# Kernel tuning notes

Hardware: AMD Instinct MI355X
Metric: run time of the kernel (lower is better)

Reference implementation:

```python
import jax, jax.numpy as jnp
import numpy as np

N_NODES = 100000
N_EDGES = 1200000
IN_DIM = 128
HID = 64
BATCH = 8192


def setup_inputs() -> dict:
    key = jax.random.key(0)
    ks = jax.random.split(key, 8)
    x = jax.random.normal(ks[0], (N_NODES, IN_DIM), dtype=jnp.float32)
    edge_index = jax.random.randint(ks[1], (2, N_EDGES), 0, N_NODES, dtype=jnp.int64)
    user_nodes = jax.random.randint(ks[2], (BATCH,), 0, N_NODES, dtype=jnp.int64)
    movie_nodes = jax.random.randint(ks[3], (BATCH,), 0, N_NODES, dtype=jnp.int64)
    # Glorot-like init for weights, zeros for biases (as in GCNConv / nn.Linear defaults)
    W1 = jax.random.normal(ks[4], (HID, IN_DIM), dtype=jnp.float32) * (1.0 / np.sqrt(IN_DIM))
    b1 = jnp.zeros((HID,), dtype=jnp.float32)
    W2 = jax.random.normal(ks[5], (HID, HID), dtype=jnp.float32) * (1.0 / np.sqrt(HID))
    b2 = jnp.zeros((HID,), dtype=jnp.float32)
    fc_w = jax.random.normal(ks[6], (1, HID), dtype=jnp.float32) * (1.0 / np.sqrt(HID))
    fc_b = jnp.zeros((1,), dtype=jnp.float32)
    return {"x": x, "edge_index": edge_index, "user_nodes": user_nodes,
            "movie_nodes": movie_nodes, "W1": W1, "b1": b1, "W2": W2, "b2": b2,
            "fc_w": fc_w, "fc_b": fc_b}


def _gcn_conv(x, src, dst, norm, W, b, n_nodes):
    # GCNConv: linear transform first, then normalized sum-aggregation, then bias.
    h = x @ W.T                                   # [N, out]
    msg = h[src] * norm[:, None]                  # gather + scale  [E+N, out]
    out = jax.ops.segment_sum(msg, dst, num_segments=n_nodes)  # scatter-add
    return out + b


def reference(x, edge_index, user_nodes, movie_nodes, W1, b1, W2, b2, fc_w, fc_b):
    n = x.shape[0]
    # add self-loops (GCNConv default add_self_loops=True)
    loop = jnp.arange(n, dtype=edge_index.dtype)
    src = jnp.concatenate([edge_index[0], loop])
    dst = jnp.concatenate([edge_index[1], loop])
    # symmetric normalization: deg computed on destination (in-degree incl. self-loop)
    deg = jax.ops.segment_sum(jnp.ones_like(src, dtype=x.dtype), dst, num_segments=n)
    dinv = jnp.where(deg > 0, jax.lax.rsqrt(deg), 0.0)
    norm = dinv[src] * dinv[dst]                  # [E+N]
    # stacked conv -> relu (dropout is identity in eval)
    h = jax.nn.relu(_gcn_conv(x, src, dst, norm, W1, b1, n))
    h = jax.nn.relu(_gcn_conv(h, src, dst, norm, W2, b2, n))
    # predict_pairs: gather, elementwise product, linear, squeeze
    interaction = h[user_nodes] * h[movie_nodes]  # [B, HID]
    scores = (interaction @ fc_w.T + fc_b)[:, 0]  # [B]
    return scores
```

## Files before the change

### kernel.cpp

```cpp
#include <hip/hip_runtime.h>

#define HID 64

#define QS1   4096.0f
#define QINV1 (1.0f/4096.0f)
#define QS2   2048.0f
#define QINV2 (1.0f/2048.0f)

__global__ void __launch_bounds__(256) hist_kernel(
    const int4* __restrict__ dst4, int* __restrict__ hist, int n4, int nblk, int nb, int epb4) {
    __shared__ int h[512];
    const int tid = threadIdx.x, blk = blockIdx.x;
    h[tid] = 0; h[tid + 256] = 0;
    __syncthreads();
    const int beg4 = blk * epb4;
    const int end4 = min(n4, beg4 + epb4);
    for (int j = beg4 + tid; j < end4; j += 256) {
        int4 d = dst4[j];
        atomicAdd(&h[d.x >> 8], 1);
        atomicAdd(&h[d.y >> 8], 1);
        atomicAdd(&h[d.z >> 8], 1);
        atomicAdd(&h[d.w >> 8], 1);
    }
    __syncthreads();
    for (int b = tid; b < nb; b += 256) hist[b * nblk + blk] = h[b];
}

__global__ void __launch_bounds__(1024) scan_partial_kernel(
    const int* __restrict__ in, int* __restrict__ tmp, int* __restrict__ bsum, int n) {
    __shared__ int sm[1024];
    const int tid = threadIdx.x;
    int i0 = blockIdx.x * 2048 + tid * 2;
    int a = (i0 < n) ? in[i0] : 0;
    int b = (i0 + 1 < n) ? in[i0 + 1] : 0;
    int v = a + b;
    sm[tid] = v;
    __syncthreads();
#pragma unroll
    for (int off = 1; off < 1024; off <<= 1) {
        int t = (tid >= off) ? sm[tid - off] : 0;
        __syncthreads();
        sm[tid] += t;
        __syncthreads();
    }
    int excl = sm[tid] - v;
    if (i0 < n) tmp[i0] = excl;
    if (i0 + 1 < n) tmp[i0 + 1] = excl + a;
    if (tid == 1023) bsum[blockIdx.x] = sm[1023];
}

__global__ void __launch_bounds__(128) scan_sums_kernel(
    const int* __restrict__ bsum, int* __restrict__ boff, int nb) {
    __shared__ int sm[128];
    const int tid = threadIdx.x;
    int v = (tid < nb) ? bsum[tid] : 0;
    sm[tid] = v;
    __syncthreads();
#pragma unroll
    for (int off = 1; off < 128; off <<= 1) {
        int t = (tid >= off) ? sm[tid - off] : 0;
        __syncthreads();
        sm[tid] += t;
        __syncthreads();
    }
    boff[tid] = sm[tid] - v;
}

__device__ __forceinline__ int scanned_at(const int* tmp, const int* boff, int idx) {
    return tmp[idx] + boff[idx >> 11];
}

__global__ void __launch_bounds__(256) partition_kernel(
    const int4* __restrict__ src4, const int4* __restrict__ dst4,
    const int* __restrict__ tmp, const int* __restrict__ boff,
    int* __restrict__ sorted, int n4, int nblk, int nb, int epb4) {
    __shared__ int cur[512];
    const int tid = threadIdx.x, blk = blockIdx.x;
    for (int b = tid; b < nb; b += 256) cur[b] = scanned_at(tmp, boff, b * nblk + blk);
    __syncthreads();
    const int beg4 = blk * epb4;
    const int end4 = min(n4, beg4 + epb4);
    for (int j = beg4 + tid; j < end4; j += 256) {
        int4 d = dst4[j];
        int4 s = src4[j];
        int p0 = atomicAdd(&cur[d.x >> 8], 1);
        int p1 = atomicAdd(&cur[d.y >> 8], 1);
        int p2 = atomicAdd(&cur[d.z >> 8], 1);
        int p3 = atomicAdd(&cur[d.w >> 8], 1);
        sorted[p0] = (s.x << 8) | (d.x & 255);
        sorted[p1] = (s.y << 8) | (d.y & 255);
        sorted[p2] = (s.z << 8) | (d.z & 255);
        sorted[p3] = (s.w << 8) | (d.w & 255);
    }
}

#define BKCAP 4096
__global__ void __launch_bounds__(256) bucket_build_kernel(
    const int* __restrict__ sorted, const int* __restrict__ tmp, const int* __restrict__ boff,
    int* __restrict__ row_ptr, float* __restrict__ dinv, int* __restrict__ col,
    int nblk, int n, int n_edges) {
    __shared__ int cnt[256], sc[256], cur[256];
    __shared__ int ecache[BKCAP];
    const int b = blockIdx.x, tid = threadIdx.x;
    const int base = scanned_at(tmp, boff, b * nblk);
    const int end  = (b == gridDim.x - 1) ? n_edges : scanned_at(tmp, boff, (b + 1) * nblk);
    const int m = end - base;
    const bool fits = (m <= BKCAP);

    cnt[tid] = 0;
    __syncthreads();
    if (fits) {
        for (int e = tid; e < m; e += 256) {
            int v = sorted[base + e];
            ecache[e] = v;
            atomicAdd(&cnt[v & 255], 1);
        }
    } else {
        for (int e = base + tid; e < end; e += 256)
            atomicAdd(&cnt[sorted[e] & 255], 1);
    }
    __syncthreads();

    sc[tid] = cnt[tid];
    __syncthreads();
#pragma unroll
    for (int off = 1; off < 256; off <<= 1) {
        int t = (tid >= off) ? sc[tid - off] : 0;
        __syncthreads();
        sc[tid] += t;
        __syncthreads();
    }
    int ex = sc[tid] - cnt[tid];
    cur[tid] = ex;

    int node = b * 256 + tid;
    if (node < n) {
        row_ptr[node] = base + ex;
        dinv[node] = rsqrtf((float)(cnt[tid] + 1));
    }
    if (b == gridDim.x - 1 && tid == 0) row_ptr[n] = n_edges;
    __syncthreads();

    if (fits) {
        for (int e = tid; e < m; e += 256) {
            int v = ecache[e];
            int lp = atomicAdd(&cur[v & 255], 1);
            col[base + lp] = v >> 8;
        }
    } else {
        for (int e = base + tid; e < end; e += 256) {
            int v = sorted[e];
            int lp = atomicAdd(&cur[v & 255], 1);
            col[base + lp] = v >> 8;
        }
    }
}

template<int K>
__global__ void __launch_bounds__(256) gemm_tile_kernel(
    const float* __restrict__ X, const float* __restrict__ W,
    const float* __restrict__ dinv, short* __restrict__ outq, float qs, int n) {
    constexpr int BK = 32;
    constexpr int NKB = K / BK;
    __shared__ float As[BK][132];
    __shared__ float Bs[BK][68];

    const int t = threadIdx.x;
    const int mbase = blockIdx.x * 128;
    const int tc = t & 15;
    const int tm = t >> 4;
    const int lr = t >> 3;
    const int k4 = (t & 7) * 4;

    float acc[8][4] = {};

    for (int kb = 0; kb < NKB; ++kb) {
        __syncthreads();
#pragma unroll
        for (int h = 0; h < 4; ++h) {
            int m = lr + h * 32;
            int node = mbase + m;
            float4 v = make_float4(0.f, 0.f, 0.f, 0.f);
            if (node < n)
                v = *reinterpret_cast<const float4*>(X + (size_t)node * K + kb * BK + k4);
            As[k4 + 0][m] = v.x; As[k4 + 1][m] = v.y;
            As[k4 + 2][m] = v.z; As[k4 + 3][m] = v.w;
        }
#pragma unroll
        for (int h = 0; h < 2; ++h) {
            int c = lr + h * 32;
            float4 wv = *reinterpret_cast<const float4*>(W + (size_t)c * K + kb * BK + k4);
            Bs[k4 + 0][c] = wv.x; Bs[k4 + 1][c] = wv.y;
            Bs[k4 + 2][c] = wv.z; Bs[k4 + 3][c] = wv.w;
        }
        __syncthreads();
#pragma unroll
        for (int k = 0; k < BK; ++k) {
            float4 a0 = *reinterpret_cast<const float4*>(&As[k][tm * 8]);
            float4 a1 = *reinterpret_cast<const float4*>(&As[k][tm * 8 + 4]);
            float4 b = *reinterpret_cast<const float4*>(&Bs[k][tc * 4]);
            acc[0][0] += a0.x * b.x; acc[0][1] += a0.x * b.y; acc[0][2] += a0.x * b.z; acc[0][3] += a0.x * b.w;
            acc[1][0] += a0.y * b.x; acc[1][1] += a0.y * b.y; acc[1][2] += a0.y * b.z; acc[1][3] += a0.y * b.w;
            acc[2][0] += a0.z * b.x; acc[2][1] += a0.z * b.y; acc[2][2] += a0.z * b.z; acc[2][3] += a0.z * b.w;
            acc[3][0] += a0.w * b.x; acc[3][1] += a0.w * b.y; acc[3][2] += a0.w * b.z; acc[3][3] += a0.w * b.w;
            acc[4][0] += a1.x * b.x; acc[4][1] += a1.x * b.y; acc[4][2] += a1.x * b.z; acc[4][3] += a1.x * b.w;
            acc[5][0] += a1.y * b.x; acc[5][1] += a1.y * b.y; acc[5][2] += a1.y * b.z; acc[5][3] += a1.y * b.w;
            acc[6][0] += a1.z * b.x; acc[6][1] += a1.z * b.y; acc[6][2] += a1.z * b.z; acc[6][3] += a1.z * b.w;
            acc[7][0] += a1.w * b.x; acc[7][1] += a1.w * b.y; acc[7][2] += a1.w * b.z; acc[7][3] += a1.w * b.w;
        }
    }

#pragma unroll
    for (int i = 0; i < 8; ++i) {
        int node = mbase + tm * 8 + i;
        if (node < n) {
            float s = dinv[node] * qs;
            int q0 = __float2int_rn(fminf(fmaxf(acc[i][0] * s, -32767.f), 32767.f));
            int q1 = __float2int_rn(fminf(fmaxf(acc[i][1] * s, -32767.f), 32767.f));
            int q2 = __float2int_rn(fminf(fmaxf(acc[i][2] * s, -32767.f), 32767.f));
            int q3 = __float2int_rn(fminf(fmaxf(acc[i][3] * s, -32767.f), 32767.f));
            int2 pk;
            pk.x = (q0 & 0xffff) | (q1 << 16);
            pk.y = (q2 & 0xffff) | (q3 << 16);
            *reinterpret_cast<int2*>(outq + (size_t)node * HID + tc * 4) = pk;
        }
    }
}

__device__ __forceinline__ float4 gather_node_q(
    const int2* __restrict__ hq, const int* __restrict__ row_ptr, const int* __restrict__ col,
    const float* __restrict__ dinv, float4 bv, float qinv, int node, int cl) {
    int beg = row_ptr[node];
    int end = row_ptr[node + 1];

    int2 sp = hq[(size_t)node * 16 + cl];
    int4 a0 = make_int4((sp.x << 16) >> 16, sp.x >> 16, (sp.y << 16) >> 16, sp.y >> 16);
    int4 a1 = make_int4(0, 0, 0, 0);
    int4 a2 = make_int4(0, 0, 0, 0);
    int4 a3 = make_int4(0, 0, 0, 0);

    int e = beg;
    for (; e + 8 <= end; e += 8) {
        int s0 = col[e], s1 = col[e + 1], s2 = col[e + 2], s3 = col[e + 3];
        int s4 = col[e + 4], s5 = col[e + 5], s6 = col[e + 6], s7 = col[e + 7];
        int2 v0 = hq[(size_t)s0 * 16 + cl];
        int2 v1 = hq[(size_t)s1 * 16 + cl];
        int2 v2 = hq[(size_t)s2 * 16 + cl];
        int2 v3 = hq[(size_t)s3 * 16 + cl];
        int2 v4 = hq[(size_t)s4 * 16 + cl];
        int2 v5 = hq[(size_t)s5 * 16 + cl];
        int2 v6 = hq[(size_t)s6 * 16 + cl];
        int2 v7 = hq[(size_t)s7 * 16 + cl];
        a0.x += (v0.x << 16) >> 16; a0.y += v0.x >> 16; a0.z += (v0.y << 16) >> 16; a0.w += v0.y >> 16;
        a1.x += (v1.x << 16) >> 16; a1.y += v1.x >> 16; a1.z += (v1.y << 16) >> 16; a1.w += v1.y >> 16;
        a2.x += (v2.x << 16) >> 16; a2.y += v2.x >> 16; a2.z += (v2.y << 16) >> 16; a2.w += v2.y >> 16;
        a3.x += (v3.x << 16) >> 16; a3.y += v3.x >> 16; a3.z += (v3.y << 16) >> 16; a3.w += v3.y >> 16;
        a0.x += (v4.x << 16) >> 16; a0.y += v4.x >> 16; a0.z += (v4.y << 16) >> 16; a0.w += v4.y >> 16;
        a1.x += (v5.x << 16) >> 16; a1.y += v5.x >> 16; a1.z += (v5.y << 16) >> 16; a1.w += v5.y >> 16;
        a2.x += (v6.x << 16) >> 16; a2.y += v6.x >> 16; a2.z += (v6.y << 16) >> 16; a2.w += v6.y >> 16;
        a3.x += (v7.x << 16) >> 16; a3.y += v7.x >> 16; a3.z += (v7.y << 16) >> 16; a3.w += v7.y >> 16;
    }
    for (; e + 4 <= end; e += 4) {
        int s0 = col[e], s1 = col[e + 1], s2 = col[e + 2], s3 = col[e + 3];
        int2 v0 = hq[(size_t)s0 * 16 + cl];
        int2 v1 = hq[(size_t)s1 * 16 + cl];
        int2 v2 = hq[(size_t)s2 * 16 + cl];
        int2 v3 = hq[(size_t)s3 * 16 + cl];
        a0.x += (v0.x << 16) >> 16; a0.y += v0.x >> 16; a0.z += (v0.y << 16) >> 16; a0.w += v0.y >> 16;
        a1.x += (v1.x << 16) >> 16; a1.y += v1.x >> 16; a1.z += (v1.y << 16) >> 16; a1.w += v1.y >> 16;
        a2.x += (v2.x << 16) >> 16; a2.y += v2.x >> 16; a2.z += (v2.y << 16) >> 16; a2.w += v2.y >> 16;
        a3.x += (v3.x << 16) >> 16; a3.y += v3.x >> 16; a3.z += (v3.y << 16) >> 16; a3.w += v3.y >> 16;
    }
    for (; e < end; ++e) {
        int2 v = hq[(size_t)col[e] * 16 + cl];
        a0.x += (v.x << 16) >> 16; a0.y += v.x >> 16; a0.z += (v.y << 16) >> 16; a0.w += v.y >> 16;
    }

    float sq = dinv[node] * qinv;
    float4 r;
    r.x = fmaf((float)((a0.x + a1.x) + (a2.x + a3.x)), sq, bv.x);
    r.y = fmaf((float)((a0.y + a1.y) + (a2.y + a3.y)), sq, bv.y);
    r.z = fmaf((float)((a0.z + a1.z) + (a2.z + a3.z)), sq, bv.z);
    r.w = fmaf((float)((a0.w + a1.w) + (a2.w + a3.w)), sq, bv.w);
    r.x = r.x > 0.f ? r.x : 0.f;
    r.y = r.y > 0.f ? r.y : 0.f;
    r.z = r.z > 0.f ? r.z : 0.f;
    r.w = r.w > 0.f ? r.w : 0.f;
    return r;
}

__global__ void __launch_bounds__(256) gather_kernel(
    const short* __restrict__ hsq, const int* __restrict__ row_ptr, const int* __restrict__ col,
    const float* __restrict__ dinv, const float* __restrict__ b, float qinv,
    float* __restrict__ out, int n) {
    const int2* __restrict__ hq = (const int2*)hsq;
    const int lane = threadIdx.x & 63;
    const int sub = lane >> 4;
    const int cl  = lane & 15;
    const int g = blockIdx.x * 4 + (threadIdx.x >> 6);

    int node = g * 4 + sub;
    if (node >= n) return;
    float4 bv = ((const float4*)b)[cl];
    float4 r = gather_node_q(hq, row_ptr, col, dinv, bv, qinv, node, cl);
    *((float4*)out + (size_t)node * 16 + cl) = r;
}

__global__ void __launch_bounds__(256) gather_sparse_kernel(
    const short* __restrict__ hsq, const int* __restrict__ row_ptr, const int* __restrict__ col,
    const int* __restrict__ users, const int* __restrict__ movies,
    const float* __restrict__ dinv, const float* __restrict__ b, float qinv,
    float* __restrict__ out, int batch) {
    const int2* __restrict__ hq = (const int2*)hsq;
    const int lane = threadIdx.x & 63;
    const int sub = lane >> 4;
    const int cl  = lane & 15;
    const int g = blockIdx.x * 4 + (threadIdx.x >> 6);

    int idx = g * 4 + sub;
    if (idx >= 2 * batch) return;
    int node = (idx < batch) ? users[idx] : movies[idx - batch];
    float4 bv = ((const float4*)b)[cl];
    float4 r = gather_node_q(hq, row_ptr, col, dinv, bv, qinv, node, cl);
    *((float4*)out + (size_t)node * 16 + cl) = r;
}

__global__ void final_kernel(const float* __restrict__ h,
                             const int* __restrict__ users, const int* __restrict__ movies,
                             const float* __restrict__ fc_w, const float* __restrict__ fc_b,
                             float* __restrict__ out, int batch) {
    const int lane = threadIdx.x & 63;
    int wid = blockIdx.x * (blockDim.x >> 6) + (threadIdx.x >> 6);
    const int nw = gridDim.x * (blockDim.x >> 6);
    for (int p = wid; p < batch; p += nw) {
        int u = users[p];
        int m = movies[p];
        float v = h[(size_t)u * HID + lane] * h[(size_t)m * HID + lane] * fc_w[lane];
#pragma unroll
        for (int off = 32; off > 0; off >>= 1)
            v += __shfl_down(v, off, 64);
        if (lane == 0) out[p] = v + fc_b[0];
    }
}

extern "C" void kernel_launch(void* const* d_in, const int* in_sizes, int n_in,
                              void* d_out, int out_size, void* d_ws, size_t ws_size,
                              hipStream_t stream) {
    const float* x     = (const float*)d_in[0];
    const int*   edge  = (const int*)d_in[1];
    const int*   users = (const int*)d_in[2];
    const int*   movies= (const int*)d_in[3];
    const float* W1    = (const float*)d_in[4];
    const float* b1    = (const float*)d_in[5];
    const float* W2    = (const float*)d_in[6];
    const float* b2    = (const float*)d_in[7];
    const float* fc_w  = (const float*)d_in[8];
    const float* fc_b  = (const float*)d_in[9];
    float* out = (float*)d_out;

    const int IN_DIM = 128;
    const int n       = in_sizes[0] / IN_DIM;
    const int n_edges = in_sizes[1] / 2;
    const int batch   = in_sizes[2];

    const int* esrc = edge;
    const int* edst = edge + n_edges;

    const int n4   = n_edges / 4;
    const int NBLK = 512;
    const int EPB4 = (n4 + NBLK - 1) / NBLK;
    const int NB   = (n + 255) >> 8;
    const int HLEN = NB * NBLK;
    const int SB   = (HLEN + 2047) / 2048;

    char* ws = (char*)d_ws;
    size_t o = 0;
    auto alloc = [&](size_t bytes) { void* p = ws + o; o = (o + bytes + 255) & ~(size_t)255; return p; };
    int*   hist    = (int*)  alloc(sizeof(int) * HLEN);
    int*   tmp     = (int*)  alloc(sizeof(int) * HLEN);
    int*   bsum    = (int*)  alloc(sizeof(int) * 128);
    int*   boff    = (int*)  alloc(sizeof(int) * 128);
    int*   sorted  = (int*)  alloc(sizeof(int) * n_edges);
    int*   col     = (int*)  alloc(sizeof(int) * n_edges);
    int*   row_ptr = (int*)  alloc(sizeof(int) * (n + 1));
    float* dinv    = (float*)alloc(sizeof(float) * n);
    short* Bq      = (short*)alloc(sizeof(short) * (size_t)n * HID);
    float* C       = (float*)alloc(sizeof(float) * (size_t)n * HID);

    hist_kernel<<<NBLK, 256, 0, stream>>>((const int4*)edst, hist, n4, NBLK, NB, EPB4);
    scan_partial_kernel<<<SB, 1024, 0, stream>>>(hist, tmp, bsum, HLEN);
    scan_sums_kernel<<<1, 128, 0, stream>>>(bsum, boff, SB);
    partition_kernel<<<NBLK, 256, 0, stream>>>((const int4*)esrc, (const int4*)edst,
                                               tmp, boff, sorted, n4, NBLK, NB, EPB4);
    bucket_build_kernel<<<NB, 256, 0, stream>>>(sorted, tmp, boff, row_ptr, dinv, col,
                                                NBLK, n, n_edges);

    const int ngroups = (n + 3) >> 2;
    const int gather_blocks = (ngroups + 3) / 4;
    const int sgroups = (2 * batch + 3) >> 2;
    const int sparse_blocks = (sgroups + 3) / 4;

    gemm_tile_kernel<128><<<(n + 127) / 128, 256, 0, stream>>>(x, W1, dinv, Bq, QS1, n);
    gather_kernel<<<gather_blocks, 256, 0, stream>>>(Bq, row_ptr, col, dinv, b1, QINV1, C, n);

    gemm_tile_kernel<64><<<(n + 127) / 128, 256, 0, stream>>>(C, W2, dinv, Bq, QS2, n);
    gather_sparse_kernel<<<sparse_blocks, 256, 0, stream>>>(Bq, row_ptr, col, users, movies,
                                                            dinv, b2, QINV2, C, batch);
    final_kernel<<<2048, 256, 0, stream>>>(C, users, movies, fc_w, fc_b, out, batch);
}
```

Measured before the change: 143.1 us.

## Quantize layer-1 output to int16 and fuse final scoring into sparse gather

The layer-1 gather now writes its ReLU output as int16 fixed point instead of fp32, and a new GEMM variant reads and dequantizes those int16 values. This halves the traffic for the intermediate hidden matrix. The layer-2 sparse gather is fused with the final dot-product head, using lane shuffles to pair each user with its movie, so the separate final kernel and the fp32 write of the hidden rows go away. The layer-1 gather also uses a fixed grid with a grid-stride loop. The extra quantization step adds rounding and clamping error to the intermediate activations.

```diff
diff --git a/kernel.cpp b/kernel.cpp
--- a/kernel.cpp
+++ b/kernel.cpp
@@ -4,6 +4,7 @@
 
 #define QS1   4096.0f
 #define QINV1 (1.0f/4096.0f)
+#define QH1   2048.0f
 #define QS2   2048.0f
 #define QINV2 (1.0f/2048.0f)
 
@@ -185,6 +186,77 @@
                 v = *reinterpret_cast<const float4*>(X + (size_t)node * K + kb * BK + k4);
             As[k4 + 0][m] = v.x; As[k4 + 1][m] = v.y;
             As[k4 + 2][m] = v.z; As[k4 + 3][m] = v.w;
+        }
+#pragma unroll
+        for (int h = 0; h < 2; ++h) {
+            int c = lr + h * 32;
+            float4 wv = *reinterpret_cast<const float4*>(W + (size_t)c * K + kb * BK + k4);
+            Bs[k4 + 0][c] = wv.x; Bs[k4 + 1][c] = wv.y;
+            Bs[k4 + 2][c] = wv.z; Bs[k4 + 3][c] = wv.w;
+        }
+        __syncthreads();
+#pragma unroll
+        for (int k = 0; k < BK; ++k) {
+            float4 a0 = *reinterpret_cast<const float4*>(&As[k][tm * 8]);
+            float4 a1 = *reinterpret_cast<const float4*>(&As[k][tm * 8 + 4]);
+            float4 b = *reinterpret_cast<const float4*>(&Bs[k][tc * 4]);
+            acc[0][0] += a0.x * b.x; acc[0][1] += a0.x * b.y; acc[0][2] += a0.x * b.z; acc[0][3] += a0.x * b.w;
+            acc[1][0] += a0.y * b.x; acc[1][1] += a0.y * b.y; acc[1][2] += a0.y * b.z; acc[1][3] += a0.y * b.w;
+            acc[2][0] += a0.z * b.x; acc[2][1] += a0.z * b.y; acc[2][2] += a0.z * b.z; acc[2][3] += a0.z * b.w;
+            acc[3][0] += a0.w * b.x; acc[3][1] += a0.w * b.y; acc[3][2] += a0.w * b.z; acc[3][3] += a0.w * b.w;
+            acc[4][0] += a1.x * b.x; acc[4][1] += a1.x * b.y; acc[4][2] += a1.x * b.z; acc[4][3] += a1.x * b.w;
+            acc[5][0] += a1.y * b.x; acc[5][1] += a1.y * b.y; acc[5][2] += a1.y * b.z; acc[5][3] += a1.y * b.w;
+            acc[6][0] += a1.z * b.x; acc[6][1] += a1.z * b.y; acc[6][2] += a1.z * b.z; acc[6][3] += a1.z * b.w;
+            acc[7][0] += a1.w * b.x; acc[7][1] += a1.w * b.y; acc[7][2] += a1.w * b.z; acc[7][3] += a1.w * b.w;
+        }
+    }
+
+#pragma unroll
+    for (int i = 0; i < 8; ++i) {
+        int node = mbase + tm * 8 + i;
+        if (node < n) {
+            float s = dinv[node] * qs;
+            int q0 = __float2int_rn(fminf(fmaxf(acc[i][0] * s, -32767.f), 32767.f));
+            int q1 = __float2int_rn(fminf(fmaxf(acc[i][1] * s, -32767.f), 32767.f));
+            int q2 = __float2int_rn(fminf(fmaxf(acc[i][2] * s, -32767.f), 32767.f));
+            int q3 = __float2int_rn(fminf(fmaxf(acc[i][3] * s, -32767.f), 32767.f));
+            int2 pk;
+            pk.x = (q0 & 0xffff) | (q1 << 16);
+            pk.y = (q2 & 0xffff) | (q3 << 16);
+            *reinterpret_cast<int2*>(outq + (size_t)node * HID + tc * 4) = pk;
+        }
+    }
+}
+
+__global__ void __launch_bounds__(256) gemm_tile_q_kernel(
+    const short* __restrict__ Xq, const float* __restrict__ W,
+    const float* __restrict__ dinv, short* __restrict__ outq, float qs, int n) {
+    constexpr int K = 64, BK = 32, NKB = 2;
+    __shared__ float As[BK][132];
+    __shared__ float Bs[BK][68];
+
+    const int t = threadIdx.x;
+    const int mbase = blockIdx.x * 128;
+    const int tc = t & 15;
+    const int tm = t >> 4;
+    const int lr = t >> 3;
+    const int k4 = (t & 7) * 4;
+
+    float acc[8][4] = {};
+
+    for (int kb = 0; kb < NKB; ++kb) {
+        __syncthreads();
+#pragma unroll
+        for (int h = 0; h < 4; ++h) {
+            int m = lr + h * 32;
+            int node = mbase + m;
+            int2 raw = make_int2(0, 0);
+            if (node < n)
+                raw = *reinterpret_cast<const int2*>(Xq + (size_t)node * K + kb * BK + k4);
+            As[k4 + 0][m] = (float)((raw.x << 16) >> 16);
+            As[k4 + 1][m] = (float)(raw.x >> 16);
+            As[k4 + 2][m] = (float)((raw.y << 16) >> 16);
+            As[k4 + 3][m] = (float)(raw.y >> 16);
         }
 #pragma unroll
         for (int h = 0; h < 2; ++h) {
@@ -291,25 +363,38 @@
 
 __global__ void __launch_bounds__(256) gather_kernel(
     const short* __restrict__ hsq, const int* __restrict__ row_ptr, const int* __restrict__ col,
-    const float* __restrict__ dinv, const float* __restrict__ b, float qinv,
-    float* __restrict__ out, int n) {
+    const float* __restrict__ dinv, const float* __restrict__ b, float qinv, float qh,
+    short* __restrict__ outq, int n) {
     const int2* __restrict__ hq = (const int2*)hsq;
     const int lane = threadIdx.x & 63;
     const int sub = lane >> 4;
     const int cl  = lane & 15;
-    const int g = blockIdx.x * 4 + (threadIdx.x >> 6);
-
-    int node = g * 4 + sub;
-    if (node >= n) return;
+    const int wv = blockIdx.x * 4 + (threadIdx.x >> 6);
+    const int nwv = gridDim.x * 4;
+    const int ngroups = (n + 3) >> 2;
+
     float4 bv = ((const float4*)b)[cl];
-    float4 r = gather_node_q(hq, row_ptr, col, dinv, bv, qinv, node, cl);
-    *((float4*)out + (size_t)node * 16 + cl) = r;
-}
-
-__global__ void __launch_bounds__(256) gather_sparse_kernel(
+
+    for (int g = wv; g < ngroups; g += nwv) {
+        int node = g * 4 + sub;
+        if (node >= n) continue;
+        float4 r = gather_node_q(hq, row_ptr, col, dinv, bv, qinv, node, cl);
+        int q0 = __float2int_rn(fminf(r.x * qh, 32767.f));
+        int q1 = __float2int_rn(fminf(r.y * qh, 32767.f));
+        int q2 = __float2int_rn(fminf(r.z * qh, 32767.f));
+        int q3 = __float2int_rn(fminf(r.w * qh, 32767.f));
+        int2 pk;
+        pk.x = (q0 & 0xffff) | (q1 << 16);
+        pk.y = (q2 & 0xffff) | (q3 << 16);
+        *((int2*)outq + (size_t)node * 16 + cl) = pk;
+    }
+}
+
+__global__ void __launch_bounds__(256) gather_final_kernel(
     const short* __restrict__ hsq, const int* __restrict__ row_ptr, const int* __restrict__ col,
     const int* __restrict__ users, const int* __restrict__ movies,
     const float* __restrict__ dinv, const float* __restrict__ b, float qinv,
+    const float* __restrict__ fc_w, const float* __restrict__ fc_b,
     float* __restrict__ out, int batch) {
     const int2* __restrict__ hq = (const int2*)hsq;
     const int lane = threadIdx.x & 63;
@@ -317,29 +402,26 @@
     const int cl  = lane & 15;
     const int g = blockIdx.x * 4 + (threadIdx.x >> 6);
 
-    int idx = g * 4 + sub;
-    if (idx >= 2 * batch) return;
-    int node = (idx < batch) ? users[idx] : movies[idx - batch];
+    int pair = g * 2 + (sub >> 1);
+    int node = 0;
+    if (pair < batch) node = ((sub & 1) == 0) ? users[pair] : movies[pair];
+
     float4 bv = ((const float4*)b)[cl];
     float4 r = gather_node_q(hq, row_ptr, col, dinv, bv, qinv, node, cl);
-    *((float4*)out + (size_t)node * 16 + cl) = r;
-}
-
-__global__ void final_kernel(const float* __restrict__ h,
-                             const int* __restrict__ users, const int* __restrict__ movies,
-                             const float* __restrict__ fc_w, const float* __restrict__ fc_b,
-                             float* __restrict__ out, int batch) {
-    const int lane = threadIdx.x & 63;
-    int wid = blockIdx.x * (blockDim.x >> 6) + (threadIdx.x >> 6);
-    const int nw = gridDim.x * (blockDim.x >> 6);
-    for (int p = wid; p < batch; p += nw) {
-        int u = users[p];
-        int m = movies[p];
-        float v = h[(size_t)u * HID + lane] * h[(size_t)m * HID + lane] * fc_w[lane];
-#pragma unroll
-        for (int off = 32; off > 0; off >>= 1)
-            v += __shfl_down(v, off, 64);
-        if (lane == 0) out[p] = v + fc_b[0];
+
+    float4 fw = ((const float4*)fc_w)[cl];
+    float px = __shfl_xor(r.x, 16, 64);
+    float py = __shfl_xor(r.y, 16, 64);
+    float pz = __shfl_xor(r.z, 16, 64);
+    float pw = __shfl_xor(r.w, 16, 64);
+    float s = r.x * px * fw.x + r.y * py * fw.y + r.z * pz * fw.z + r.w * pw * fw.w;
+#pragma unroll
+    for (int off = 1; off < 16; off <<= 1)
+        s += __shfl_xor(s, off, 64);
+
+    if ((lane & 31) == 0) {
+        int pr = g * 2 + (lane >> 5);
+        if (pr < batch) out[pr] = s + fc_b[0];
     }
 }
 
@@ -385,7 +467,7 @@
     int*   row_ptr = (int*)  alloc(sizeof(int) * (n + 1));
     float* dinv    = (float*)alloc(sizeof(float) * n);
     short* Bq      = (short*)alloc(sizeof(short) * (size_t)n * HID);
-    float* C       = (float*)alloc(sizeof(float) * (size_t)n * HID);
+    short* Hq      = (short*)alloc(sizeof(short) * (size_t)n * HID);
 
     hist_kernel<<<NBLK, 256, 0, stream>>>((const int4*)edst, hist, n4, NBLK, NB, EPB4);
     scan_partial_kernel<<<SB, 1024, 0, stream>>>(hist, tmp, bsum, HLEN);
@@ -395,16 +477,16 @@
     bucket_build_kernel<<<NB, 256, 0, stream>>>(sorted, tmp, boff, row_ptr, dinv, col,
                                                 NBLK, n, n_edges);
 
-    const int ngroups = (n + 3) >> 2;
-    const int gather_blocks = (ngroups + 3) / 4;
-    const int sgroups = (2 * batch + 3) >> 2;
-    const int sparse_blocks = (sgroups + 3) / 4;
+    const int gather_blocks = 3125;
+    const int head_blocks = (batch + 7) / 8;
 
     gemm_tile_kernel<128><<<(n + 127) / 128, 256, 0, stream>>>(x, W1, dinv, Bq, QS1, n);
-    gather_kernel<<<gather_blocks, 256, 0, stream>>>(Bq, row_ptr, col, dinv, b1, QINV1, C, n);
-
-    gemm_tile_kernel<64><<<(n + 127) / 128, 256, 0, stream>>>(C, W2, dinv, Bq, QS2, n);
-    gather_sparse_kernel<<<sparse_blocks, 256, 0, stream>>>(Bq, row_ptr, col, users, movies,
-                                                            dinv, b2, QINV2, C, batch);
-    final_kernel<<<2048, 256, 0, stream>>>(C, users, movies, fc_w, fc_b, out, batch);
-}
+    gather_kernel<<<gather_blocks, 256, 0, stream>>>(Bq, row_ptr, col, dinv, b1,
+                                                     QINV1, QH1, Hq, n);
+
+    gemm_tile_q_kernel<<<(n + 127) / 128, 256, 0, stream>>>(Hq, W2, dinv, Bq, QS2 / QH1, n);
+    gather_final_kernel<<<head_blocks, 256, 0, stream>>>(Bq, row_ptr, col, users, movies,
+                                                         dinv, b2, QINV2, fc_w, fc_b,
+                                                         out, batch);
+
+}
```

Result: no change. 145.4 us (+1.6%).
